# Kernel optimization log

Measured on AMD Instinct MI355X. Metric: run time of the kernel, lower is better.

The kernel has to match this reference:

```python
import jax, jax.numpy as jnp
import numpy as np

B, TK, NK, H, E, V = 128, 400, 50, 256, 256, 50000


def setup_inputs() -> dict:
    key = jax.random.key(0)
    ks = iter(jax.random.split(key, 48))
    def rn(shape, s=1.0):
        return jax.random.normal(next(ks), shape, jnp.float32) * s
    def ru(shape):
        return jax.random.uniform(next(ks), shape, jnp.float32)
    z = lambda shape: jnp.zeros(shape, jnp.float32)
    s = 0.05
    inp = {}
    inp['y_t_1'] = jax.random.randint(next(ks), (B,), 0, V)
    inp['h_prev'] = rn((B, H))
    inp['c_prev'] = rn((B, H))
    inp['encoder_outputs'] = rn((B, TK, H))
    inp['encoder_outputs_node'] = rn((B, NK, H))
    inp['enc_padding_mask'] = jnp.ones((B, TK), jnp.float32)
    inp['enc_padding_mask_node'] = jnp.ones((B, NK), jnp.float32)
    inp['c_t_d'] = rn((B, H))
    inp['c_t_g'] = rn((B, H))
    inp['c_t_g2'] = rn((B, H))
    inp['coverage'] = z((B, TK))
    inp['flow'] = ru((B, NK))
    inp['node_to_token'] = ru((B, NK, TK))
    inp['graph'] = ru((B, NK, NK))
    inp['voc_d'] = jax.random.randint(next(ks), (B, TK), 0, V)
    inp['step'] = 0
    # learned parameters
    inp['emb_table'] = rn((V, E), s)
    inp['Wx'] = rn((4 * H, E), s); inp['bx'] = z((E,))
    inp['Wi'] = rn((E, 4 * H), s); inp['Wh'] = rn((H, 4 * H), s)
    inp['bi'] = z((4 * H,)); inp['bh'] = z((4 * H,))
    inp['Whd'] = rn((H, H), s); inp['Wsd'] = rn((2 * H, H), s)
    inp['wcd'] = rn((H,), s); inp['vd'] = rn((H,), s); inp['bd'] = z((H,))
    inp['Wn'] = rn((H, H), s); inp['Wsf'] = rn((2 * H, H), s)
    inp['vf'] = rn((H,), s); inp['bf'] = z((H,))
    inp['Wpg'] = rn((5 * H + E, 1), s); inp['bpg'] = z((1,))
    inp['W1'] = rn((4 * H, H), s); inp['b1'] = z((H,))
    inp['W2'] = rn((H, V), s); inp['b2'] = z((V,))
    return inp


def _forward(y_t_1, h_prev, c_prev, enc, enc_n, mask_t, mask_n, c_t_d, c_t_g, c_t_g2,
             coverage, flow, n2t, graph, voc_d, emb_table, Wx, bx, Wi, Wh, bi, bh,
             Whd, Wsd, wcd, vd, bd, Wn, Wsf, vf, bf, Wpg, bpg, W1, b1, W2, b2):
    sig, tanh = jax.nn.sigmoid, jnp.tanh
    y_emb = emb_table[y_t_1]                                   # [B,E]
    x = jnp.concatenate([c_t_d, c_t_g, c_t_g2, y_emb], 1) @ Wx + bx
    # single-step LSTM (torch gate order i,f,g,o)
    gates = x @ Wi + h_prev @ Wh + bi + bh
    gi, gf, gg, go = jnp.split(gates, 4, axis=1)
    c_new = sig(gf) * c_prev + sig(gi) * tanh(gg)
    h_new = sig(go) * tanh(c_new)
    s_hat = jnp.concatenate([h_new, c_new], 1)                 # [B,2H]
    # doc attention with coverage (Bahdanau)
    e = tanh(enc @ Whd + (s_hat @ Wsd)[:, None, :] + coverage[:, :, None] * wcd + bd) @ vd
    a = jax.nn.softmax(e, axis=1) * mask_t
    a = a / a.sum(1, keepdims=True)                            # [B,TK]
    c_d = jnp.einsum('bt,bth->bh', a, enc)
    coverage_next = coverage + a
    # event-graph node attention (flow-weighted, one-hop propagation)
    en = tanh(enc_n @ Wn + (s_hat @ Wsf)[:, None, :] + bf) @ vf
    an = jax.nn.softmax(en, axis=1) * mask_n
    an = an / an.sum(1, keepdims=True)
    an = an * flow
    an = an / an.sum(1, keepdims=True)                         # [B,NK]
    c_g = jnp.einsum('bn,bnh->bh', an, enc_n)
    an2 = jnp.einsum('bn,bnm->bm', an, graph) * mask_n
    an2 = an2 / an2.sum(1, keepdims=True)
    c_g2 = jnp.einsum('bn,bnh->bh', an2, enc_n)
    a_n2t = jnp.einsum('bn,bnt->bt', an, n2t)
    a_n2t = a_n2t / a_n2t.sum(1, keepdims=True)
    # flow update: per-node max of token attention restricted to node tokens
    flow_ = jnp.max(a[:, None, :] * n2t, axis=2)               # [B,NK]
    flow_next = flow_ / flow_.sum(1, keepdims=True)
    # pointer-generator gate
    p_gen = sig(jnp.concatenate([c_d, c_g, c_g2, s_hat, x], 1) @ Wpg + bpg)  # [B,1]
    out = jnp.concatenate([h_new, c_d, c_g, c_g2], 1) @ W1 + b1
    vocab_dist = jax.nn.softmax(out @ W2 + b2, axis=1)         # [B,V]
    attn_all = a / a.sum(1, keepdims=True)
    attn_ = (1.0 - p_gen) * attn_all
    vocab_ = p_gen * vocab_dist
    rows = jnp.arange(vocab_.shape[0])[:, None]
    final_dist = vocab_.at[rows, voc_d].add(attn_)             # scatter_add over vocab
    return (final_dist, (h_new, c_new), c_d, c_g, c_g2, a, a_n2t, p_gen,
            coverage_next, flow_next)


def reference(y_t_1, h_prev, c_prev, encoder_outputs, encoder_outputs_node,
              enc_padding_mask, enc_padding_mask_node, c_t_d, c_t_g, c_t_g2,
              coverage, flow, node_to_token, graph, voc_d, step,
              emb_table, Wx, bx, Wi, Wh, bi, bh, Whd, Wsd, wcd, vd, bd,
              Wn, Wsf, vf, bf, Wpg, bpg, W1, b1, W2, b2):
    return _forward(y_t_1, h_prev, c_prev, encoder_outputs, encoder_outputs_node,
                    enc_padding_mask, enc_padding_mask_node, c_t_d, c_t_g, c_t_g2,
                    coverage, flow, node_to_token, graph, voc_d, emb_table, Wx, bx,
                    Wi, Wh, bi, bh, Whd, Wsd, wcd, vd, bd, Wn, Wsf, vf, bf,
                    Wpg, bpg, W1, b1, W2, b2)
```

## Files before the change

### kernel.cpp

```cpp
#include <hip/hip_runtime.h>
#include <stdint.h>


typedef unsigned short u16;
typedef unsigned int   u32;

#define Bv  128
#define TKv 400
#define NKv 50
#define Hv  256
#define Vv  50000
#define VPAD 50176
#define NSv 16
#define CHUNKv 3136
#define MDOC (Bv * TKv)
#define MNODE (Bv * NKv)

typedef __attribute__((ext_vector_type(8))) short bf16x8;
typedef __attribute__((ext_vector_type(4))) float f32x4;

__device__ float g_x[32768];
__device__ float g_xp[4 * 32768];
__device__ float g_gates[131072];
__device__ float g_h[32768];
__device__ float g_c[32768];
__device__ float g_sdp[2 * 32768];
__device__ float g_sfp[2 * 32768];
__device__ float g_ep[4 * MDOC];
__device__ float g_enp[4 * MNODE];
__device__ float g_a[51200];
__device__ float g_cd[32768];
__device__ float g_cdp[8 * 32768];
__device__ float g_cg[32768];
__device__ float g_cg2[32768];
__device__ float g_pg[128];
__device__ float g_o1[32768];
__device__ __attribute__((aligned(16))) u16 g_o1b[32768];
__device__ float g_vred[Bv * NSv * 2];
__device__ float g_logits[6400000];
__device__ u16   g_Wdt[256 * 256];
__device__ u16   g_Wnt[256 * 256];
__device__ u16   g_W2t[(size_t)VPAD * 256];
__device__ u16   g_encb[(size_t)Bv * TKv * 256];
__device__ u16   g_encnb[(size_t)Bv * NKv * 256];

__device__ __forceinline__ float sigm(float x) { return 1.f / (1.f + expf(-x)); }

__device__ __forceinline__ u16 f2bf(float f) {
    u32 u = __float_as_uint(f);
    return (u16)((u + 0x7fffu + ((u >> 16) & 1u)) >> 16);
}

__device__ __forceinline__ bf16x8 cvt8(const float* __restrict__ p) {
    const float4 a = *(const float4*)p;
    const float4 b = *(const float4*)(p + 4);
    bf16x8 r;
    r[0] = (short)f2bf(a.x); r[1] = (short)f2bf(a.y);
    r[2] = (short)f2bf(a.z); r[3] = (short)f2bf(a.w);
    r[4] = (short)f2bf(b.x); r[5] = (short)f2bf(b.y);
    r[6] = (short)f2bf(b.z); r[7] = (short)f2bf(b.w);
    return r;
}

__device__ __forceinline__ float fast_tanh(float x) {
    x = fminf(fmaxf(x, -15.f), 15.f);
    float e = __expf(2.f * x);
    return (e - 1.f) / (e + 1.f);
}

__device__ __forceinline__ void ms_merge(float& m1, float& s1, float m2, float s2) {
    float M = fmaxf(m1, m2);
    s1 = s1 * expf(m1 - M) + s2 * expf(m2 - M);
    m1 = M;
}

__global__ __launch_bounds__(256) void k_cvt(
    const float* __restrict__ src, u16* __restrict__ dst, int n8)
{
    int i = blockIdx.x * 256 + threadIdx.x;
    const int stride = gridDim.x * 256;
    for (; i < n8; i += stride)
        *(bf16x8*)(dst + (size_t)i * 8) = cvt8(src + (size_t)i * 8);
}

__global__ __launch_bounds__(256) void k_tc(
    const float* __restrict__ src, u16* __restrict__ dst, int K, int N)
{
    __shared__ float tile[32][33];
    const int n0 = blockIdx.x * 32, k0 = blockIdx.y * 32;
    const int tx = threadIdx.x & 31, ty = threadIdx.x >> 5;
    #pragma unroll
    for (int i = 0; i < 32; i += 8) {
        int k = k0 + ty + i, n = n0 + tx;
        tile[ty + i][tx] = (n < N) ? src[(size_t)k * N + n] : 0.f;
    }
    __syncthreads();
    #pragma unroll
    for (int i = 0; i < 32; i += 8) {
        int n = n0 + ty + i, k = k0 + tx;
        dst[(size_t)n * K + k] = f2bf(tile[tx][ty + i]);
    }
}

__global__ __launch_bounds__(256) void k_x(
    const int* __restrict__ y,
    const float* __restrict__ ctd, const float* __restrict__ ctg,
    const float* __restrict__ ctg2, const float* __restrict__ emb,
    const float* __restrict__ Wx)
{
    const int b = blockIdx.x, ks = blockIdx.y, j = threadIdx.x;
    __shared__ float cs[256];
    float v;
    if      (ks == 0) v = ctd [b * 256 + j];
    else if (ks == 1) v = ctg [b * 256 + j];
    else if (ks == 2) v = ctg2[b * 256 + j];
    else              v = emb[(size_t)y[b] * 256 + j];
    cs[j] = v;
    __syncthreads();

    float acc = 0.f;
    const float* w = Wx + (size_t)(ks * 256) * 256 + j;
    #pragma unroll 8
    for (int k = 0; k < 256; k++) acc += cs[k] * w[(size_t)k * 256];
    g_xp[ks * 32768 + b * 256 + j] = acc;
}

__global__ __launch_bounds__(256) void k_gates(
    const float* __restrict__ h_prev,
    const float* __restrict__ Wi, const float* __restrict__ Wh,
    const float* __restrict__ bi, const float* __restrict__ bh,
    const float* __restrict__ bx)
{
    const int b = blockIdx.x, cc = blockIdx.y, j = threadIdx.x;
    __shared__ float xs[256], hs[256];

    float xv = bx[j] + g_xp[b * 256 + j] + g_xp[32768 + b * 256 + j]
             + g_xp[65536 + b * 256 + j] + g_xp[98304 + b * 256 + j];
    xs[j] = xv;
    if (cc == 0) g_x[b * 256 + j] = xv;
    hs[j] = h_prev[b * 256 + j];
    __syncthreads();

    const int col = cc * 256 + j;
    float acc = bi[col] + bh[col];
    const float* wi = Wi + col;
    const float* wh = Wh + col;
    #pragma unroll 8
    for (int k = 0; k < 256; k++)
        acc += xs[k] * wi[(size_t)k * 1024] + hs[k] * wh[(size_t)k * 1024];
    g_gates[b * 1024 + col] = acc;
}

__global__ __launch_bounds__(256) void k_cellsd(
    const float* __restrict__ c_prev,
    const float* __restrict__ Wsd, const float* __restrict__ Wsf,
    float* __restrict__ out_h, float* __restrict__ out_c)
{
    const int b = blockIdx.x, ks = blockIdx.y, j = threadIdx.x;
    __shared__ float sh[256];

    const float* gb = g_gates + b * 1024;
    float gi_ = gb[j], gf_ = gb[256 + j], gg_ = gb[512 + j], go_ = gb[768 + j];
    float cp = c_prev[b * 256 + j];
    float cn = sigm(gf_) * cp + sigm(gi_) * tanhf(gg_);
    float hn = sigm(go_) * tanhf(cn);
    if (ks == 0) {
        g_h[b * 256 + j] = hn;  g_c[b * 256 + j] = cn;
        out_h[b * 256 + j] = hn; out_c[b * 256 + j] = cn;
    }
    sh[j] = (ks == 0) ? hn : cn;
    __syncthreads();

    float asd = 0.f, asf = 0.f;
    const float* wd = Wsd + (size_t)(ks * 256) * 256 + j;
    const float* wf = Wsf + (size_t)(ks * 256) * 256 + j;
    #pragma unroll 8
    for (int k = 0; k < 256; k++) {
        float sv = sh[k];
        asd += sv * wd[(size_t)k * 256];
        asf += sv * wf[(size_t)k * 256];
    }
    g_sdp[ks * 32768 + b * 256 + j] = asd;
    g_sfp[ks * 32768 + b * 256 + j] = asf;
}

template<int R>
__global__ __launch_bounds__(256) void k_scores(
    const u16* __restrict__ srcb,
    const u16* __restrict__ Wt,
    const float* __restrict__ addv0,
    const float* __restrict__ addv1,
    const float* __restrict__ abias,
    const float* __restrict__ cov,
    const float* __restrict__ wcw,
    const float* __restrict__ vv,
    float* __restrict__ eout, int Mtot)
{
    const int tid = threadIdx.x;
    const int lane = tid & 63, w = tid >> 6;
    const int nlow = lane & 15, quad = lane >> 4;
    const int c0 = blockIdx.y * 64;

    __shared__ u16 Bs[64][264];
    {
        const u16* wsrc = Wt + (size_t)c0 * 256;
        #pragma unroll
        for (int j = 0; j < 8; j++) {
            int chunk = tid + j * 256;
            int row = chunk >> 5, c16 = chunk & 31;
            *(bf16x8*)(&Bs[row][c16 * 8]) =
                *(const bf16x8*)(wsrc + row * 256 + c16 * 8);
        }
    }
    __syncthreads();

    const int rowbase = blockIdx.x * 128 + w * 32;
    const u16* a0 = srcb + (size_t)(rowbase + nlow) * 256 + quad * 8;
    const u16* a1 = a0 + 16 * 256;

    const f32x4 zf = {0.f, 0.f, 0.f, 0.f};
    f32x4 acc[2][4];
    #pragma unroll
    for (int mi = 0; mi < 2; mi++)
        #pragma unroll
        for (int ni = 0; ni < 4; ni++) acc[mi][ni] = zf;

    bf16x8 af0 = *(const bf16x8*)(a0);
    bf16x8 af1 = *(const bf16x8*)(a1);
    for (int k0 = 0; k0 < 256; k0 += 32) {
        const int kn = (k0 + 32) & 255;
        bf16x8 nf0 = *(const bf16x8*)(a0 + kn);
        bf16x8 nf1 = *(const bf16x8*)(a1 + kn);
        bf16x8 bf[4];
        #pragma unroll
        for (int ni = 0; ni < 4; ni++)
            bf[ni] = *(const bf16x8*)(&Bs[ni * 16 + nlow][k0 + quad * 8]);
        #pragma unroll
        for (int ni = 0; ni < 4; ni++) {
            acc[0][ni] = __builtin_amdgcn_mfma_f32_16x16x32_bf16(af0, bf[ni], acc[0][ni], 0, 0, 0);
            acc[1][ni] = __builtin_amdgcn_mfma_f32_16x16x32_bf16(af1, bf[ni], acc[1][ni], 0, 0, 0);
        }
        af0 = nf0; af1 = nf1;
    }

    #pragma unroll
    for (int mi = 0; mi < 2; mi++) {
        float covt[4]; int bidx[4];
        #pragma unroll
        for (int r = 0; r < 4; r++) {
            int row = rowbase + mi * 16 + quad * 4 + r;
            covt[r] = cov ? cov[row] : 0.f;
            bidx[r] = row / R;
        }
        float s4[4] = {0.f, 0.f, 0.f, 0.f};
        #pragma unroll
        for (int ni = 0; ni < 4; ni++) {
            int col = c0 + ni * 16 + nlow;
            float vvc = vv[col];
            float ab  = abias[col];
            float wcc = wcw ? wcw[col] : 0.f;
            #pragma unroll
            for (int r = 0; r < 4; r++) {
                float adc = addv0[bidx[r] * 256 + col] + addv1[bidx[r] * 256 + col] + ab;
                s4[r] += vvc * fast_tanh(acc[mi][ni][r] + adc + covt[r] * wcc);
            }
        }
        #pragma unroll
        for (int r = 0; r < 4; r++) {
            float s = s4[r];
            s += __shfl_xor(s, 1, 64);
            s += __shfl_xor(s, 2, 64);
            s += __shfl_xor(s, 4, 64);
            s += __shfl_xor(s, 8, 64);
            int row = rowbase + mi * 16 + quad * 4 + r;
            if (nlow == 0)
                eout[(size_t)blockIdx.y * Mtot + row] = s;
        }
    }
}

__global__ __launch_bounds__(256) void k_doc(
    const float* __restrict__ mask,
    const float* __restrict__ cov,
    float* __restrict__ out_a, float* __restrict__ out_cov)
{
    const int b = blockIdx.x, tid = threadIdx.x;
    __shared__ float red[256];

    float e0 = 0.f, e1s = 0.f;
    #pragma unroll
    for (int ch = 0; ch < 4; ch++) {
        e0 += g_ep[ch * MDOC + b * TKv + tid];
        if (tid + 256 < TKv) e1s += g_ep[ch * MDOC + b * TKv + tid + 256];
    }
    float e1 = (tid + 256 < TKv) ? e1s : -1e30f;

    float m = fmaxf(e0, e1);
    red[tid] = m; __syncthreads();
    for (int s = 128; s > 0; s >>= 1) { if (tid < s) red[tid] = fmaxf(red[tid], red[tid + s]); __syncthreads(); }
    m = red[0]; __syncthreads();

    float p0 = expf(e0 - m) * mask[b * TKv + tid];
    float p1 = (tid + 256 < TKv) ? expf(e1 - m) * mask[b * TKv + tid + 256] : 0.f;
    red[tid] = p0 + p1; __syncthreads();
    for (int s = 128; s > 0; s >>= 1) { if (tid < s) red[tid] += red[tid + s]; __syncthreads(); }
    float inv = 1.f / red[0];

    float a0 = p0 * inv;
    g_a[b * TKv + tid] = a0;
    out_a[b * TKv + tid] = a0;
    out_cov[b * TKv + tid] = cov[b * TKv + tid] + a0;
    if (tid + 256 < TKv) {
        float a1 = p1 * inv;
        g_a[b * TKv + tid + 256] = a1;
        out_a[b * TKv + tid + 256] = a1;
        out_cov[b * TKv + tid + 256] = cov[b * TKv + tid + 256] + a1;
    }
}

__global__ __launch_bounds__(256) void k_cd(const float* __restrict__ enc)
{
    const int b = blockIdx.x, ks = blockIdx.y, tid = threadIdx.x;
    __shared__ float as_[50];
    if (tid < 50) as_[tid] = g_a[b * TKv + ks * 50 + tid];
    __syncthreads();

    const float* eb = enc + ((size_t)b * TKv + ks * 50) * 256 + tid;
    float acc = 0.f;
    #pragma unroll 10
    for (int t = 0; t < 50; t++) acc += as_[t] * eb[(size_t)t * 256];
    g_cdp[ks * 32768 + b * 256 + tid] = acc;
}

__global__ __launch_bounds__(256) void k_flow(
    const float* __restrict__ n2t, float* __restrict__ out_flow)
{
    const int b = blockIdx.x, tid = threadIdx.x;
    __shared__ float as_[TKv];
    __shared__ float fl[NKv];
    __shared__ float red[256];

    for (int t = tid; t < TKv; t += 256) as_[t] = g_a[b * TKv + t];
    __syncthreads();

    const int nn = tid >> 2, sub = tid & 3;
    float mx = 0.f;
    if (nn < NKv) {
        const float* nb = n2t + ((size_t)b * NKv + nn) * TKv + sub * 100;
        const float* ab = as_ + sub * 100;
        #pragma unroll 4
        for (int t = 0; t < 100; t++) mx = fmaxf(mx, ab[t] * nb[t]);
    }
    mx = fmaxf(mx, __shfl_xor(mx, 1, 64));
    mx = fmaxf(mx, __shfl_xor(mx, 2, 64));
    if (sub == 0 && nn < NKv) fl[nn] = mx;
    __syncthreads();

    float fv = (tid < NKv) ? fl[tid] : 0.f;
    red[tid] = fv; __syncthreads();
    for (int s = 128; s > 0; s >>= 1) { if (tid < s) red[tid] += red[tid + s]; __syncthreads(); }
    float fs = red[0];
    if (tid < NKv) out_flow[b * NKv + tid] = fl[tid] / fs;
}

__global__ __launch_bounds__(256) void k_node1(
    const float* __restrict__ encn,
    const float* __restrict__ maskn,
    const float* __restrict__ flow,
    const float* __restrict__ graph,
    const float* __restrict__ n2t,
    const float* __restrict__ Wpg, const float* __restrict__ bpg,
    float* __restrict__ out_cd, float* __restrict__ out_cg,
    float* __restrict__ out_cg2, float* __restrict__ out_ant,
    float* __restrict__ out_pgen)
{
    const int b = blockIdx.x, tid = threadIdx.x;
    __shared__ float ans[NKv], an2s[NKv], red[256];

    float cd = 0.f;
    #pragma unroll
    for (int i = 0; i < 8; i++) cd += g_cdp[i * 32768 + b * 256 + tid];
    g_cd[b * 256 + tid] = cd;
    out_cd[b * 256 + tid] = cd;

    float v = -1e30f;
    if (tid < NKv) {
        v = 0.f;
        #pragma unroll
        for (int ch = 0; ch < 4; ch++) v += g_enp[ch * MNODE + b * NKv + tid];
    }
    red[tid] = v; __syncthreads();
    for (int s = 128; s > 0; s >>= 1) { if (tid < s) red[tid] = fmaxf(red[tid], red[tid + s]); __syncthreads(); }
    float m = red[0]; __syncthreads();

    float p = (tid < NKv) ? expf(v - m) * maskn[b * NKv + tid] : 0.f;
    red[tid] = p; __syncthreads();
    for (int s = 128; s > 0; s >>= 1) { if (tid < s) red[tid] += red[tid + s]; __syncthreads(); }
    float S = red[0]; __syncthreads();
    p = (tid < NKv) ? (p / S) * flow[b * NKv + tid] : 0.f;
    red[tid] = p; __syncthreads();
    for (int s = 128; s > 0; s >>= 1) { if (tid < s) red[tid] += red[tid + s]; __syncthreads(); }
    float S2 = red[0]; __syncthreads();
    if (tid < NKv) ans[tid] = p / S2;
    __syncthreads();

    float q = 0.f;
    if (tid < NKv) {
        const float* gb = graph + (size_t)b * NKv * NKv + tid;
        #pragma unroll
        for (int n = 0; n < NKv; n++) q += ans[n] * gb[n * NKv];
        q *= maskn[b * NKv + tid];
    }
    red[tid] = q; __syncthreads();
    for (int s = 128; s > 0; s >>= 1) { if (tid < s) red[tid] += red[tid + s]; __syncthreads(); }
    float S3 = red[0]; __syncthreads();
    if (tid < NKv) an2s[tid] = q / S3;
    __syncthreads();

    float cg = 0.f, cg2 = 0.f;
    {
        const float* enb = encn + (size_t)b * NKv * 256 + tid;
        #pragma unroll
        for (int n = 0; n < NKv; n++) {
            float e = enb[n * 256];
            cg  += ans[n]  * e;
            cg2 += an2s[n] * e;
        }
    }
    g_cg[b * 256 + tid] = cg;   out_cg[b * 256 + tid] = cg;
    g_cg2[b * 256 + tid] = cg2; out_cg2[b * 256 + tid] = cg2;

    float at0 = 0.f, at1 = 0.f;
    {
        const float* nb = n2t + (size_t)b * NKv * TKv;
        #pragma unroll
        for (int n = 0; n < NKv; n++) {
            float an = ans[n];
            at0 += an * nb[n * TKv + tid];
            if (tid + 256 < TKv) at1 += an * nb[n * TKv + tid + 256];
        }
    }
    float loc = at0 + ((tid + 256 < TKv) ? at1 : 0.f);
    red[tid] = loc; __syncthreads();
    for (int s = 128; s > 0; s >>= 1) { if (tid < s) red[tid] += red[tid + s]; __syncthreads(); }
    float S4 = red[0]; __syncthreads();
    out_ant[b * TKv + tid] = at0 / S4;
    if (tid + 256 < TKv) out_ant[b * TKv + tid + 256] = at1 / S4;

    float hvv = g_h[b * 256 + tid], cvv = g_c[b * 256 + tid];
    float xvv = g_x[b * 256 + tid];
    float part = cd  * Wpg[tid]        + cg  * Wpg[256 + tid]
               + cg2 * Wpg[512 + tid]  + hvv * Wpg[768 + tid]
               + cvv * Wpg[1024 + tid] + xvv * Wpg[1280 + tid];
    red[tid] = part; __syncthreads();
    for (int s = 128; s > 0; s >>= 1) { if (tid < s) red[tid] += red[tid + s]; __syncthreads(); }
    if (tid == 0) {
        float pg = sigm(red[0] + bpg[0]);
        g_pg[b] = pg; out_pgen[b] = pg;
    }
}

__global__ __launch_bounds__(256) void k_o1(
    const float* __restrict__ W1, const float* __restrict__ b1)
{
    const int b = blockIdx.x, cc = blockIdx.y, tid = threadIdx.x;
    __shared__ float cat[1024];
    __shared__ float red[256];

    cat[tid]       = g_h  [b * 256 + tid];
    cat[256 + tid] = g_cd [b * 256 + tid];
    cat[512 + tid] = g_cg [b * 256 + tid];
    cat[768 + tid] = g_cg2[b * 256 + tid];
    __syncthreads();

    const int lane = tid & 63, kq = tid >> 6;
    const int col = cc * 64 + lane;
    const float* w  = W1 + (size_t)(kq * 256) * 256 + col;
    const float* cs = cat + kq * 256;
    float acc = 0.f;
    #pragma unroll 8
    for (int k = 0; k < 256; k++) acc += cs[k] * w[(size_t)k * 256];
    red[tid] = acc; __syncthreads();

    if (tid < 64) {
        float o = b1[cc * 64 + tid]
                + red[tid] + red[64 + tid] + red[128 + tid] + red[192 + tid];
        g_o1[b * 256 + cc * 64 + tid] = o;
        g_o1b[b * 256 + cc * 64 + tid] = f2bf(o);
    }
}

__global__ __launch_bounds__(256) void k_logits(const float* __restrict__ b2)
{
    const int v0 = blockIdx.x * 64;
    const int tid = threadIdx.x;
    const int lane = tid & 63, wave = tid >> 6;
    const int nlow = lane & 15, quad = lane >> 4;

    const u16* a0p = g_o1b + (wave * 32 + nlow) * 256 + quad * 8;
    const u16* a1p = a0p + 16 * 256;
    const u16* bbase = g_W2t + (size_t)(v0 + nlow) * 256 + quad * 8;

    const f32x4 zf = {0.f, 0.f, 0.f, 0.f};
    f32x4 acc0[4], acc1[4];
    #pragma unroll
    for (int i = 0; i < 4; i++) { acc0[i] = zf; acc1[i] = zf; }

    for (int k0 = 0; k0 < 256; k0 += 32) {
        bf16x8 a0 = *(const bf16x8*)(a0p + k0);
        bf16x8 a1 = *(const bf16x8*)(a1p + k0);
        #pragma unroll
        for (int nt = 0; nt < 4; nt++) {
            bf16x8 bf = *(const bf16x8*)(bbase + (size_t)nt * 4096 + k0);
            acc0[nt] = __builtin_amdgcn_mfma_f32_16x16x32_bf16(a0, bf, acc0[nt], 0, 0, 0);
            acc1[nt] = __builtin_amdgcn_mfma_f32_16x16x32_bf16(a1, bf, acc1[nt], 0, 0, 0);
        }
    }

    #pragma unroll
    for (int nt = 0; nt < 4; nt++) {
        int v = v0 + nt * 16 + nlow;
        if (v < Vv) {
            float bb = b2[v];
            #pragma unroll
            for (int r = 0; r < 4; r++) {
                int row0 = wave * 32 + quad * 4 + r;
                g_logits[(size_t)row0 * Vv + v]        = acc0[nt][r] + bb;
                g_logits[(size_t)(row0 + 16) * Vv + v] = acc1[nt][r] + bb;
            }
        }
    }
}

__global__ __launch_bounds__(256) void k_vpart()
{
    const int b = blockIdx.x, ks = blockIdx.y, tid = threadIdx.x;
    __shared__ float rm[256], rs[256];

    const int base = ks * CHUNKv;
    const int end  = min(base + CHUNKv, Vv);
    const int n4   = (end - base) >> 2;
    const float4* L4 = (const float4*)(g_logits + (size_t)b * Vv + base);

    float m = -1e30f, s = 0.f;
    for (int i = tid; i < n4; i += 256) {
        float4 x = L4[i];
        float mx = fmaxf(fmaxf(x.x, x.y), fmaxf(x.z, x.w));
        if (mx > m) { s *= expf(m - mx); m = mx; }
        s += expf(x.x - m) + expf(x.y - m) + expf(x.z - m) + expf(x.w - m);
    }
    rm[tid] = m; rs[tid] = s; __syncthreads();
    for (int off = 128; off > 0; off >>= 1) {
        if (tid < off) {
            float m1 = rm[tid], s1 = rs[tid];
            ms_merge(m1, s1, rm[tid + off], rs[tid + off]);
            rm[tid] = m1; rs[tid] = s1;
        }
        __syncthreads();
    }
    if (tid == 0) {
        g_vred[(b * NSv + ks) * 2]     = rm[0];
        g_vred[(b * NSv + ks) * 2 + 1] = rs[0];
    }
}

__global__ __launch_bounds__(256) void k_vwrite(float* __restrict__ outF)
{
    const int b = blockIdx.x, ks = blockIdx.y, tid = threadIdx.x;

    float M = -1e30f, S = 0.f;
    #pragma unroll
    for (int i = 0; i < NSv; i++) {
        float mi = g_vred[(b * NSv + i) * 2];
        float si = g_vred[(b * NSv + i) * 2 + 1];
        ms_merge(M, S, mi, si);
    }
    const float inv = g_pg[b] / S;

    const int base = ks * CHUNKv;
    const int end  = min(base + CHUNKv, Vv);
    const int n4   = (end - base) >> 2;
    const float4* L4 = (const float4*)(g_logits + (size_t)b * Vv + base);
    float4* O4 = (float4*)(outF + (size_t)b * Vv + base);

    for (int i = tid; i < n4; i += 256) {
        float4 x = L4[i];
        float4 r;
        r.x = expf(x.x - M) * inv;
        r.y = expf(x.y - M) * inv;
        r.z = expf(x.z - M) * inv;
        r.w = expf(x.w - M) * inv;
        O4[i] = r;
    }
}

__global__ __launch_bounds__(256) void k_scatter(
    float* __restrict__ outF, const int* __restrict__ vocd)
{
    const int b = blockIdx.x, tid = threadIdx.x;
    float* Ob = outF + (size_t)b * Vv;
    const float omp = 1.f - g_pg[b];
    for (int t = tid; t < TKv; t += 256)
        atomicAdd(Ob + vocd[b * TKv + t], omp * g_a[b * TKv + t]);
}


extern "C" void kernel_launch(void* const* d_in, const int* in_sizes, int n_in,
                              void* d_out, int out_size, void* d_ws, size_t ws_size,
                              hipStream_t stream)
{
    (void)in_sizes; (void)n_in; (void)out_size; (void)d_ws; (void)ws_size;

    const int*   y      = (const int*)d_in[0];
    const float* h_prev = (const float*)d_in[1];
    const float* c_prev = (const float*)d_in[2];
    const float* enc    = (const float*)d_in[3];
    const float* encn   = (const float*)d_in[4];
    const float* mask   = (const float*)d_in[5];
    const float* maskn  = (const float*)d_in[6];
    const float* ctd    = (const float*)d_in[7];
    const float* ctg    = (const float*)d_in[8];
    const float* ctg2   = (const float*)d_in[9];
    const float* cov    = (const float*)d_in[10];
    const float* flow   = (const float*)d_in[11];
    const float* n2t    = (const float*)d_in[12];
    const float* graph  = (const float*)d_in[13];
    const int*   vocd   = (const int*)d_in[14];
    const float* emb    = (const float*)d_in[16];
    const float* Wx     = (const float*)d_in[17];
    const float* bx     = (const float*)d_in[18];
    const float* Wi     = (const float*)d_in[19];
    const float* Wh     = (const float*)d_in[20];
    const float* bi     = (const float*)d_in[21];
    const float* bh     = (const float*)d_in[22];
    const float* Whd    = (const float*)d_in[23];
    const float* Wsd    = (const float*)d_in[24];
    const float* wcdw   = (const float*)d_in[25];
    const float* vd     = (const float*)d_in[26];
    const float* bd     = (const float*)d_in[27];
    const float* Wn     = (const float*)d_in[28];
    const float* Wsf    = (const float*)d_in[29];
    const float* vf     = (const float*)d_in[30];
    const float* bfv    = (const float*)d_in[31];
    const float* Wpg    = (const float*)d_in[32];
    const float* bpg    = (const float*)d_in[33];
    const float* W1     = (const float*)d_in[34];
    const float* b1     = (const float*)d_in[35];
    const float* W2     = (const float*)d_in[36];
    const float* b2     = (const float*)d_in[37];

    float* o = (float*)d_out;
    float* o_final = o;
    float* o_h     = o + 6400000;
    float* o_c     = o + 6432768;
    float* o_cd    = o + 6465536;
    float* o_cg    = o + 6498304;
    float* o_cg2   = o + 6531072;
    float* o_a     = o + 6563840;
    float* o_ant   = o + 6615040;
    float* o_pg    = o + 6666240;
    float* o_cov   = o + 6666368;
    float* o_fl    = o + 6717568;

    float* g_ep_p;  hipGetSymbolAddress((void**)&g_ep_p,  HIP_SYMBOL(g_ep));
    float* g_enp_p; hipGetSymbolAddress((void**)&g_enp_p, HIP_SYMBOL(g_enp));
    float* g_sdp_p; hipGetSymbolAddress((void**)&g_sdp_p, HIP_SYMBOL(g_sdp));
    float* g_sfp_p; hipGetSymbolAddress((void**)&g_sfp_p, HIP_SYMBOL(g_sfp));
    u16*   g_Wdt_p; hipGetSymbolAddress((void**)&g_Wdt_p, HIP_SYMBOL(g_Wdt));
    u16*   g_Wnt_p; hipGetSymbolAddress((void**)&g_Wnt_p, HIP_SYMBOL(g_Wnt));
    u16*   g_W2t_p; hipGetSymbolAddress((void**)&g_W2t_p, HIP_SYMBOL(g_W2t));
    u16*   g_encb_p;  hipGetSymbolAddress((void**)&g_encb_p,  HIP_SYMBOL(g_encb));
    u16*   g_encnb_p; hipGetSymbolAddress((void**)&g_encnb_p, HIP_SYMBOL(g_encnb));

    k_tc<<<dim3(8, 8), dim3(256), 0, stream>>>(Whd, g_Wdt_p, 256, 256);
    k_tc<<<dim3(8, 8), dim3(256), 0, stream>>>(Wn,  g_Wnt_p, 256, 256);
    k_tc<<<dim3(VPAD / 32, 8), dim3(256), 0, stream>>>(W2, g_W2t_p, 256, Vv);

    k_cvt<<<dim3(2048), dim3(256), 0, stream>>>(enc,  g_encb_p,  Bv * TKv * 256 / 8);
    k_cvt<<<dim3(800),  dim3(256), 0, stream>>>(encn, g_encnb_p, Bv * NKv * 256 / 8);

    k_x<<<dim3(Bv, 4), dim3(256), 0, stream>>>(y, ctd, ctg, ctg2, emb, Wx);

    k_gates<<<dim3(Bv, 4), dim3(256), 0, stream>>>(h_prev, Wi, Wh, bi, bh, bx);

    k_cellsd<<<dim3(Bv, 2), dim3(256), 0, stream>>>(c_prev, Wsd, Wsf, o_h, o_c);

    k_scores<TKv><<<dim3(MDOC / 128, 4), dim3(256), 0, stream>>>(
        g_encb_p, g_Wdt_p, g_sdp_p, g_sdp_p + 32768, bd, cov, wcdw, vd,
        g_ep_p, MDOC);

    k_scores<NKv><<<dim3(MNODE / 128, 4), dim3(256), 0, stream>>>(
        g_encnb_p, g_Wnt_p, g_sfp_p, g_sfp_p + 32768, bfv,
        nullptr, nullptr, vf, g_enp_p, MNODE);

    k_doc<<<dim3(Bv), dim3(256), 0, stream>>>(mask, cov, o_a, o_cov);

    k_cd<<<dim3(Bv, 8), dim3(256), 0, stream>>>(enc);

    k_flow<<<dim3(Bv), dim3(256), 0, stream>>>(n2t, o_fl);

    k_node1<<<dim3(Bv), dim3(256), 0, stream>>>(
        encn, maskn, flow, graph, n2t, Wpg, bpg,
        o_cd, o_cg, o_cg2, o_ant, o_pg);

    k_o1<<<dim3(Bv, 4), dim3(256), 0, stream>>>(W1, b1);

    k_logits<<<dim3(VPAD / 64), dim3(256), 0, stream>>>(b2);

    k_vpart<<<dim3(Bv, NSv), dim3(256), 0, stream>>>();

    k_vwrite<<<dim3(Bv, NSv), dim3(256), 0, stream>>>(o_final);

    k_scatter<<<dim3(Bv), dim3(256), 0, stream>>>(o_final, vocd);
}
```

Before: 481.6 us.

## Fuse softmax partials into logits GEMM epilogue and parallelize flow/ant kernels

```diff
diff --git a/kernel.cpp b/kernel.cpp
--- a/kernel.cpp
+++ b/kernel.cpp
@@ -15,6 +15,7 @@
 #define CHUNKv 3136
 #define MDOC (Bv * TKv)
 #define MNODE (Bv * NKv)
+#define NBLK (VPAD / 64)
 
 typedef __attribute__((ext_vector_type(8))) short bf16x8;
 typedef __attribute__((ext_vector_type(4))) float f32x4;
@@ -34,9 +35,14 @@
 __device__ float g_cg[32768];
 __device__ float g_cg2[32768];
 __device__ float g_pg[128];
+__device__ float g_ans[MNODE];
+__device__ float g_inv4[128];
+__device__ float g_fl[MNODE];
+__device__ float g_nrs[MNODE];
 __device__ float g_o1[32768];
 __device__ __attribute__((aligned(16))) u16 g_o1b[32768];
-__device__ float g_vred[Bv * NSv * 2];
+__device__ float g_vpp[(size_t)2 * Bv * NBLK];
+__device__ float g_vred[Bv * 2];
 __device__ float g_logits[6400000];
 __device__ u16   g_Wdt[256 * 256];
 __device__ u16   g_Wnt[256 * 256];
@@ -332,35 +338,47 @@
     g_cdp[ks * 32768 + b * 256 + tid] = acc;
 }
 
-__global__ __launch_bounds__(256) void k_flow(
-    const float* __restrict__ n2t, float* __restrict__ out_flow)
+__global__ __launch_bounds__(256) void k_fmax(const float* __restrict__ n2t)
+{
+    const int bn = blockIdx.x;
+    const int b = bn / NKv;
+    const int tid = threadIdx.x;
+    __shared__ float rmx[256], rsm[256];
+
+    const float* nb = n2t + (size_t)bn * TKv;
+    const float* ab = g_a + b * TKv;
+
+    float x0 = nb[tid], a0 = ab[tid];
+    float mx = a0 * x0, sm = x0;
+    if (tid + 256 < TKv) {
+        float x1 = nb[tid + 256], a1 = ab[tid + 256];
+        mx = fmaxf(mx, a1 * x1);
+        sm += x1;
+    }
+    mx = fmaxf(mx, 0.f);
+    rmx[tid] = mx; rsm[tid] = sm; __syncthreads();
+    for (int s = 128; s > 0; s >>= 1) {
+        if (tid < s) {
+            rmx[tid] = fmaxf(rmx[tid], rmx[tid + s]);
+            rsm[tid] += rsm[tid + s];
+        }
+        __syncthreads();
+    }
+    if (tid == 0) { g_fl[bn] = rmx[0]; g_nrs[bn] = rsm[0]; }
+}
+
+__global__ __launch_bounds__(64) void k_flow2(float* __restrict__ out_flow)
 {
     const int b = blockIdx.x, tid = threadIdx.x;
-    __shared__ float as_[TKv];
-    __shared__ float fl[NKv];
-    __shared__ float red[256];
-
-    for (int t = tid; t < TKv; t += 256) as_[t] = g_a[b * TKv + t];
-    __syncthreads();
-
-    const int nn = tid >> 2, sub = tid & 3;
-    float mx = 0.f;
-    if (nn < NKv) {
-        const float* nb = n2t + ((size_t)b * NKv + nn) * TKv + sub * 100;
-        const float* ab = as_ + sub * 100;
-        #pragma unroll 4
-        for (int t = 0; t < 100; t++) mx = fmaxf(mx, ab[t] * nb[t]);
-    }
-    mx = fmaxf(mx, __shfl_xor(mx, 1, 64));
-    mx = fmaxf(mx, __shfl_xor(mx, 2, 64));
-    if (sub == 0 && nn < NKv) fl[nn] = mx;
-    __syncthreads();
-
-    float fv = (tid < NKv) ? fl[tid] : 0.f;
-    red[tid] = fv; __syncthreads();
-    for (int s = 128; s > 0; s >>= 1) { if (tid < s) red[tid] += red[tid + s]; __syncthreads(); }
-    float fs = red[0];
-    if (tid < NKv) out_flow[b * NKv + tid] = fl[tid] / fs;
+    float v = (tid < NKv) ? g_fl[b * NKv + tid] : 0.f;
+    float s = v;
+    s += __shfl_xor(s, 1, 64);
+    s += __shfl_xor(s, 2, 64);
+    s += __shfl_xor(s, 4, 64);
+    s += __shfl_xor(s, 8, 64);
+    s += __shfl_xor(s, 16, 64);
+    s += __shfl_xor(s, 32, 64);
+    if (tid < NKv) out_flow[b * NKv + tid] = v / s;
 }
 
 __global__ __launch_bounds__(256) void k_node1(
@@ -368,11 +386,9 @@
     const float* __restrict__ maskn,
     const float* __restrict__ flow,
     const float* __restrict__ graph,
-    const float* __restrict__ n2t,
     const float* __restrict__ Wpg, const float* __restrict__ bpg,
     float* __restrict__ out_cd, float* __restrict__ out_cg,
-    float* __restrict__ out_cg2, float* __restrict__ out_ant,
-    float* __restrict__ out_pgen)
+    float* __restrict__ out_cg2, float* __restrict__ out_pgen)
 {
     const int b = blockIdx.x, tid = threadIdx.x;
     __shared__ float ans[NKv], an2s[NKv], red[256];
@@ -401,7 +417,16 @@
     red[tid] = p; __syncthreads();
     for (int s = 128; s > 0; s >>= 1) { if (tid < s) red[tid] += red[tid + s]; __syncthreads(); }
     float S2 = red[0]; __syncthreads();
-    if (tid < NKv) ans[tid] = p / S2;
+    if (tid < NKv) {
+        ans[tid] = p / S2;
+        g_ans[b * NKv + tid] = ans[tid];
+    }
+    __syncthreads();
+
+    float s4p = (tid < NKv) ? ans[tid] * g_nrs[b * NKv + tid] : 0.f;
+    red[tid] = s4p; __syncthreads();
+    for (int s = 128; s > 0; s >>= 1) { if (tid < s) red[tid] += red[tid + s]; __syncthreads(); }
+    if (tid == 0) g_inv4[b] = 1.f / red[0];
     __syncthreads();
 
     float q = 0.f;
@@ -429,23 +454,6 @@
     }
     g_cg[b * 256 + tid] = cg;   out_cg[b * 256 + tid] = cg;
     g_cg2[b * 256 + tid] = cg2; out_cg2[b * 256 + tid] = cg2;
-
-    float at0 = 0.f, at1 = 0.f;
-    {
-        const float* nb = n2t + (size_t)b * NKv * TKv;
-        #pragma unroll
-        for (int n = 0; n < NKv; n++) {
-            float an = ans[n];
-            at0 += an * nb[n * TKv + tid];
-            if (tid + 256 < TKv) at1 += an * nb[n * TKv + tid + 256];
-        }
-    }
-    float loc = at0 + ((tid + 256 < TKv) ? at1 : 0.f);
-    red[tid] = loc; __syncthreads();
-    for (int s = 128; s > 0; s >>= 1) { if (tid < s) red[tid] += red[tid + s]; __syncthreads(); }
-    float S4 = red[0]; __syncthreads();
-    out_ant[b * TKv + tid] = at0 / S4;
-    if (tid + 256 < TKv) out_ant[b * TKv + tid + 256] = at1 / S4;
 
     float hvv = g_h[b * 256 + tid], cvv = g_c[b * 256 + tid];
     float xvv = g_x[b * 256 + tid];
@@ -460,6 +468,24 @@
     }
 }
 
+__global__ __launch_bounds__(256) void k_ant(
+    const float* __restrict__ n2t, float* __restrict__ out_ant)
+{
+    const int b = blockIdx.x, ks = blockIdx.y, tid = threadIdx.x;
+    __shared__ float ans[NKv];
+    if (tid < NKv) ans[tid] = g_ans[b * NKv + tid];
+    __syncthreads();
+
+    if (tid < 200) {
+        const int t = ks * 200 + tid;
+        const float* nb = n2t + (size_t)b * NKv * TKv + t;
+        float at = 0.f;
+        #pragma unroll
+        for (int n = 0; n < NKv; n++) at += ans[n] * nb[n * TKv];
+        out_ant[b * TKv + t] = at * g_inv4[b];
+    }
+}
+
 __global__ __launch_bounds__(256) void k_o1(
     const float* __restrict__ W1, const float* __restrict__ b1)
 {
@@ -517,39 +543,55 @@
         }
     }
 
+    float bbv[4]; bool val[4];
     #pragma unroll
     for (int nt = 0; nt < 4; nt++) {
         int v = v0 + nt * 16 + nlow;
-        if (v < Vv) {
-            float bb = b2[v];
+        val[nt] = v < Vv;
+        bbv[nt] = val[nt] ? b2[v] : 0.f;
+    }
+
+    #pragma unroll
+    for (int mi = 0; mi < 2; mi++) {
+        #pragma unroll
+        for (int r = 0; r < 4; r++) {
+            const int row = wave * 32 + mi * 16 + quad * 4 + r;
+            float x[4];
             #pragma unroll
-            for (int r = 0; r < 4; r++) {
-                int row0 = wave * 32 + quad * 4 + r;
-                g_logits[(size_t)row0 * Vv + v]        = acc0[nt][r] + bb;
-                g_logits[(size_t)(row0 + 16) * Vv + v] = acc1[nt][r] + bb;
+            for (int nt = 0; nt < 4; nt++) {
+                float xv = (mi ? acc1[nt][r] : acc0[nt][r]) + bbv[nt];
+                if (val[nt]) g_logits[(size_t)row * Vv + v0 + nt * 16 + nlow] = xv;
+                x[nt] = val[nt] ? xv : -1e30f;
             }
-        }
-    }
-}
-
-__global__ __launch_bounds__(256) void k_vpart()
-{
-    const int b = blockIdx.x, ks = blockIdx.y, tid = threadIdx.x;
+            float m = fmaxf(fmaxf(x[0], x[1]), fmaxf(x[2], x[3]));
+            m = fmaxf(m, __shfl_xor(m, 1, 64));
+            m = fmaxf(m, __shfl_xor(m, 2, 64));
+            m = fmaxf(m, __shfl_xor(m, 4, 64));
+            m = fmaxf(m, __shfl_xor(m, 8, 64));
+            float s = expf(x[0] - m) + expf(x[1] - m)
+                    + expf(x[2] - m) + expf(x[3] - m);
+            s += __shfl_xor(s, 1, 64);
+            s += __shfl_xor(s, 2, 64);
+            s += __shfl_xor(s, 4, 64);
+            s += __shfl_xor(s, 8, 64);
+            if (nlow == 0) {
+                g_vpp[((size_t)row * NBLK + blockIdx.x) * 2]     = m;
+                g_vpp[((size_t)row * NBLK + blockIdx.x) * 2 + 1] = s;
+            }
+        }
+    }
+}
+
+__global__ __launch_bounds__(256) void k_vmerge()
+{
+    const int b = blockIdx.x, tid = threadIdx.x;
     __shared__ float rm[256], rs[256];
 
-    const int base = ks * CHUNKv;
-    const int end  = min(base + CHUNKv, Vv);
-    const int n4   = (end - base) >> 2;
-    const float4* L4 = (const float4*)(g_logits + (size_t)b * Vv + base);
-
-    float m = -1e30f, s = 0.f;
-    for (int i = tid; i < n4; i += 256) {
-        float4 x = L4[i];
-        float mx = fmaxf(fmaxf(x.x, x.y), fmaxf(x.z, x.w));
-        if (mx > m) { s *= expf(m - mx); m = mx; }
-        s += expf(x.x - m) + expf(x.y - m) + expf(x.z - m) + expf(x.w - m);
-    }
-    rm[tid] = m; rs[tid] = s; __syncthreads();
+    float M = -1e30f, S = 0.f;
+    for (int i = tid; i < NBLK; i += 256)
+        ms_merge(M, S, g_vpp[((size_t)b * NBLK + i) * 2],
+                       g_vpp[((size_t)b * NBLK + i) * 2 + 1]);
+    rm[tid] = M; rs[tid] = S; __syncthreads();
     for (int off = 128; off > 0; off >>= 1) {
         if (tid < off) {
             float m1 = rm[tid], s1 = rs[tid];
@@ -558,24 +600,15 @@
         }
         __syncthreads();
     }
-    if (tid == 0) {
-        g_vred[(b * NSv + ks) * 2]     = rm[0];
-        g_vred[(b * NSv + ks) * 2 + 1] = rs[0];
-    }
+    if (tid == 0) { g_vred[b * 2] = rm[0]; g_vred[b * 2 + 1] = rs[0]; }
 }
 
 __global__ __launch_bounds__(256) void k_vwrite(float* __restrict__ outF)
 {
     const int b = blockIdx.x, ks = blockIdx.y, tid = threadIdx.x;
 
-    float M = -1e30f, S = 0.f;
-    #pragma unroll
-    for (int i = 0; i < NSv; i++) {
-        float mi = g_vred[(b * NSv + i) * 2];
-        float si = g_vred[(b * NSv + i) * 2 + 1];
-        ms_merge(M, S, mi, si);
-    }
-    const float inv = g_pg[b] / S;
+    const float M = g_vred[b * 2];
+    const float inv = g_pg[b] / g_vred[b * 2 + 1];
 
     const int base = ks * CHUNKv;
     const int end  = min(base + CHUNKv, Vv);
@@ -695,19 +728,23 @@
 
     k_doc<<<dim3(Bv), dim3(256), 0, stream>>>(mask, cov, o_a, o_cov);
 
+    k_fmax<<<dim3(Bv * NKv), dim3(256), 0, stream>>>(n2t);
+
+    k_flow2<<<dim3(Bv), dim3(64), 0, stream>>>(o_fl);
+
     k_cd<<<dim3(Bv, 8), dim3(256), 0, stream>>>(enc);
 
-    k_flow<<<dim3(Bv), dim3(256), 0, stream>>>(n2t, o_fl);
-
     k_node1<<<dim3(Bv), dim3(256), 0, stream>>>(
-        encn, maskn, flow, graph, n2t, Wpg, bpg,
-        o_cd, o_cg, o_cg2, o_ant, o_pg);
+        encn, maskn, flow, graph, Wpg, bpg,
+        o_cd, o_cg, o_cg2, o_pg);
+
+    k_ant<<<dim3(Bv, 2), dim3(256), 0, stream>>>(n2t, o_ant);
 
     k_o1<<<dim3(Bv, 4), dim3(256), 0, stream>>>(W1, b1);
 
-    k_logits<<<dim3(VPAD / 64), dim3(256), 0, stream>>>(b2);
-
-    k_vpart<<<dim3(Bv, NSv), dim3(256), 0, stream>>>();
+    k_logits<<<dim3(NBLK), dim3(256), 0, stream>>>(b2);
+
+    k_vmerge<<<dim3(Bv), dim3(256), 0, stream>>>();
 
     k_vwrite<<<dim3(Bv, NSv), dim3(256), 0, stream>>>(o_final);
 
```

Result: faster. 466.8 us (-3.1%).
